# Optimization experiments

Hardware: AMD Instinct MI355X
Metric: run time of the kernel (lower is better)

The kernel has to match this reference:

```python
import jax, jax.numpy as jnp
import numpy as np

TAU, LBDA, THETA = 0.25, 0.15, 0.3
N_WARPS, N_ITERS = 1, 30
EPS = 1e-12  # GRAD_IS_ZERO

GAUSS = jnp.array([
    [0.000874, 0.006976, 0.01386, 0.006976, 0.000874],
    [0.006976, 0.0557, 0.110656, 0.0557, 0.006976],
    [0.01386, 0.110656, 0.219833, 0.110656, 0.01386],
    [0.006976, 0.0557, 0.110656, 0.0557, 0.006976],
    [0.000874, 0.006976, 0.01386, 0.006976, 0.000874]], dtype=jnp.float32)


def to_gray(x):  # [B,3,H,W] -> [B,1,H,W], BGR-style weights from repo
    w = jnp.array([0.114, 0.587, 0.299], x.dtype)
    return jnp.einsum('bchw,c->bhw', x, w)[:, None]


def normalize_pair(x1, x2):
    mn = jnp.minimum(x1.min(), x2.min())
    mx = jnp.maximum(x1.max(), x2.max())
    den = mx - mn
    return 255.0 * (x1 - mn) / den, 255.0 * (x2 - mn) / den


def gaussian_smooth(x):
    k = GAUSS[None, None].astype(x.dtype)
    return jax.lax.conv_general_dilated(x, k, (1, 1), 'SAME')


def centered_grad(x):  # central differences, one-sided at borders (scaled 0.5)
    dx = jnp.concatenate([0.5 * (x[..., 1:2] - x[..., 0:1]),
                          0.5 * (x[..., 2:] - x[..., :-2]),
                          0.5 * (x[..., -1:] - x[..., -2:-1])], axis=-1)
    dy = jnp.concatenate([0.5 * (x[..., 1:2, :] - x[..., 0:1, :]),
                          0.5 * (x[..., 2:, :] - x[..., :-2, :]),
                          0.5 * (x[..., -1:, :] - x[..., -2:-1, :])], axis=-2)
    return dx, dy


def fwd_grad(x):  # forward differences, zero at last col/row
    dx = jnp.concatenate([x[..., 1:] - x[..., :-1], jnp.zeros_like(x[..., :1])], axis=-1)
    dy = jnp.concatenate([x[..., 1:, :] - x[..., :-1, :], jnp.zeros_like(x[..., :1, :])], axis=-2)
    return dx, dy


def divergence(px, py):  # adjoint of fwd_grad (backward differences with boundary handling)
    xp = jnp.concatenate([jnp.zeros_like(px[..., :1]), px[..., :-1]], axis=-1)
    yp = jnp.concatenate([jnp.zeros_like(py[..., :1, :]), py[..., :-1, :]], axis=-2)
    dx = jnp.concatenate([xp[..., 1:] - xp[..., :-1], -xp[..., -1:]], axis=-1)
    dy = jnp.concatenate([yp[..., 1:, :] - yp[..., :-1, :], -yp[..., -1:, :]], axis=-2)
    return dx + dy


def warp(x, u, v):  # grid_sample bilinear, align_corners=True, zeros padding
    B, C, H, W = x.shape
    base_x = jnp.linspace(-1.0, 1.0, W)[None, None, :]
    base_y = jnp.linspace(-1.0, 1.0, H)[None, :, None]
    gx = base_x + 2.0 * u[:, 0] / W   # [B,H,W]
    gy = base_y + 2.0 * v[:, 0] / H
    ix = (gx + 1.0) * 0.5 * (W - 1)
    iy = (gy + 1.0) * 0.5 * (H - 1)
    ix0 = jnp.floor(ix); iy0 = jnp.floor(iy)
    wx = ix - ix0; wy = iy - iy0

    def gather(yy, xx):
        valid = (xx >= 0) & (xx <= W - 1) & (yy >= 0) & (yy <= H - 1)
        xi = jnp.clip(xx, 0, W - 1).astype(jnp.int32)
        yi = jnp.clip(yy, 0, H - 1).astype(jnp.int32)
        flat = (yi * W + xi).reshape(B, 1, H * W)
        g = jnp.take_along_axis(x.reshape(B, C, H * W), flat, axis=2).reshape(B, C, H, W)
        return g * valid[:, None].astype(x.dtype)

    return (gather(iy0, ix0) * ((1 - wx) * (1 - wy))[:, None]
            + gather(iy0, ix0 + 1) * (wx * (1 - wy))[:, None]
            + gather(iy0 + 1, ix0) * ((1 - wx) * wy)[:, None]
            + gather(iy0 + 1, ix0 + 1) * (wx * wy)[:, None])


def tvnet_scale(x1, x2, u1, u2):
    l_t = LBDA * THETA
    taut = TAU / THETA
    d2x, d2y = centered_grad(x2)
    p11 = jnp.zeros_like(x1); p12 = jnp.zeros_like(x1)
    p21 = jnp.zeros_like(x1); p22 = jnp.zeros_like(x1)
    rho = jnp.zeros_like(x1)
    for _ in range(N_WARPS):
        x2w = warp(x2, u1, u2)
        dxw = warp(d2x, u1, u2)
        dyw = warp(d2y, u1, u2)
        grad = dxw ** 2 + dyw ** 2 + EPS
        rho_c = x2w - dxw * u1 - dyw * u2 - x1

        def body(carry, _):
            u1, u2, p11, p12, p21, p22, _ = carry
            rho = rho_c + dxw * u1 + dyw * u2 + EPS
            th = l_t * grad
            m3 = (rho >= -th) & (rho <= th) & (grad > EPS)
            coef = (jnp.where(rho < -th, l_t, 0.0)
                    + jnp.where(rho > th, -l_t, 0.0)
                    + jnp.where(m3, -rho / grad, 0.0))
            v1 = coef * dxw + u1
            v2 = coef * dyw + u2
            u1n = v1 + THETA * divergence(p11, p12)
            u2n = v2 + THETA * divergence(p21, p22)
            u1x, u1y = fwd_grad(u1n)
            u2x, u2y = fwd_grad(u2n)
            ng1 = 1.0 + taut * jnp.sqrt(u1x ** 2 + u1y ** 2 + EPS)
            ng2 = 1.0 + taut * jnp.sqrt(u2x ** 2 + u2y ** 2 + EPS)
            p11n = (p11 + taut * u1x) / ng1
            p12n = (p12 + taut * u1y) / ng1
            p21n = (p21 + taut * u2x) / ng2
            p22n = (p22 + taut * u2y) / ng2
            return (u1n, u2n, p11n, p12n, p21n, p22n, rho), None

        (u1, u2, p11, p12, p21, p22, rho), _ = jax.lax.scan(
            body, (u1, u2, p11, p12, p21, p22, rho), None, length=N_ITERS)
    return u1, u2, rho


def setup_inputs() -> dict:
    key = jax.random.key(0)
    k1, k2 = jax.random.split(key)
    x1 = jax.random.uniform(k1, (8, 3, 256, 256), dtype=jnp.float32)
    x2 = jax.random.uniform(k2, (8, 3, 256, 256), dtype=jnp.float32)
    return {"x1": x1, "x2": x2}


def reference(x1, x2):
    g1 = to_gray(x1)
    g2 = to_gray(x2)
    n1, n2 = normalize_pair(g1, g2)
    s1 = gaussian_smooth(n1)
    s2 = gaussian_smooth(n2)
    u1 = jnp.zeros_like(s1)
    u2 = jnp.zeros_like(s1)
    u1, u2, rho = tvnet_scale(s1, s2, u1, u2)
    return jnp.concatenate([u1, u2, rho], axis=1)  # [B,3,H,W]
```

## Files before the change

kernel.cpp:

```cpp
#include <hip/hip_runtime.h>
#include <math.h>

typedef float v2f __attribute__((ext_vector_type(2)));
static __device__ __forceinline__ v2f v2(float a, float b){ v2f r; r.x=a; r.y=b; return r; }
#define PKFMA(a,b,c) __builtin_elementwise_fma((a),(b),(c))

#define HH 256
#define WW 256
#define BB 8
#define NPIX (BB*HH*WW)
#define HWPLANE (HH*WW)
#define EPSF 1e-12f

#define TS 32
#define HL 10
#define SS (TS + 2*HL)
#define SS2 (SS*SS)
#define NTH 1024
#define NC 3

#define GSS (TS + 6)
#define GSS2 (GSS*GSS)
#define S2S (TS + 2)
#define S2S2 (S2S*S2S)

constexpr float L_T   = (float)(0.15*0.3);
constexpr float TAUT  = (float)(0.25/0.3);
constexpr float THETA = 0.3f;

static __device__ __constant__ float GK[25] = {
  0.000874f, 0.006976f, 0.01386f,  0.006976f, 0.000874f,
  0.006976f, 0.0557f,   0.110656f, 0.0557f,   0.006976f,
  0.01386f,  0.110656f, 0.219833f, 0.110656f, 0.01386f,
  0.006976f, 0.0557f,   0.110656f, 0.0557f,   0.006976f,
  0.000874f, 0.006976f, 0.01386f,  0.006976f, 0.000874f };


__global__ void k_gray_minmax(const float* __restrict__ x1, const float* __restrict__ x2,
                              float* __restrict__ g1, float* __restrict__ g2,
                              unsigned int* __restrict__ mnmx) {
    __shared__ float smn[4], smx[4];
    float mn = 1e30f, mx = -1e30f;
    int stride = gridDim.x * blockDim.x;
    const int NV = 2*NPIX/4;
    for (int v = blockIdx.x*blockDim.x + threadIdx.x; v < NV; v += stride) {
        int img = v >> 17;
        int rem = v & (NPIX/4 - 1);
        const float* x = img ? x2 : x1;
        float* g = img ? g2 : g1;
        int b = rem >> 14;
        int pix = (rem & (HWPLANE/4 - 1)) << 2;
        const float* base = x + (size_t)b*3*HWPLANE + pix;
        float4 c0 = *(const float4*)(base);
        float4 c1 = *(const float4*)(base + HWPLANE);
        float4 c2 = *(const float4*)(base + 2*HWPLANE);
        float4 gr;
        gr.x = 0.114f*c0.x + 0.587f*c1.x + 0.299f*c2.x;
        gr.y = 0.114f*c0.y + 0.587f*c1.y + 0.299f*c2.y;
        gr.z = 0.114f*c0.z + 0.587f*c1.z + 0.299f*c2.z;
        gr.w = 0.114f*c0.w + 0.587f*c1.w + 0.299f*c2.w;
        *(float4*)(g + ((size_t)rem << 2)) = gr;
        mn = fminf(mn, fminf(fminf(gr.x, gr.y), fminf(gr.z, gr.w)));
        mx = fmaxf(mx, fmaxf(fmaxf(gr.x, gr.y), fmaxf(gr.z, gr.w)));
    }
    #pragma unroll
    for (int off = 32; off; off >>= 1) {
        mn = fminf(mn, __shfl_down(mn, off, 64));
        mx = fmaxf(mx, __shfl_down(mx, off, 64));
    }
    int wid = threadIdx.x >> 6;
    if ((threadIdx.x & 63) == 0) { smn[wid] = mn; smx[wid] = mx; }
    __syncthreads();
    if (threadIdx.x == 0) {
        mn = fminf(fminf(smn[0], smn[1]), fminf(smn[2], smn[3]));
        mx = fmaxf(fmaxf(smx[0], smx[1]), fmaxf(smx[2], smx[3]));
        atomicMin(&mnmx[0], __float_as_uint(mn));
        atomicMax((int*)&mnmx[1], (int)__float_as_uint(mx));
    }
}

__global__ void __launch_bounds__(256)
k_smooth_grad(const float* __restrict__ g1, const float* __restrict__ g2,
              const unsigned int* __restrict__ mnmx, float4* __restrict__ dxr) {
    __shared__ float gn1[GSS2], gn2[GSS2], s2L[S2S2];
    const int blk   = blockIdx.x;
    const int plane = blk >> 6;
    const int t     = blk & 63;
    const int oy0   = (t >> 3) << 5;
    const int ox0   = (t & 7) << 5;
    const int pbse  = plane * HWPLANE;
    const int tid   = threadIdx.x;

    const float mn  = __uint_as_float(mnmx[0]);
    const float inv = 255.0f / (__uint_as_float(mnmx[1]) - mn);

    for (int s = tid; s < GSS2; s += 256) {
        int sy = s / GSS, sx = s - sy*GSS;
        int gy = oy0 - 3 + sy, gx = ox0 - 3 + sx;
        bool im = (gx >= 0) & (gx < WW) & (gy >= 0) & (gy < HH);
        int gi = pbse + gy*WW + gx;
        gn1[s] = im ? (g1[gi] - mn)*inv : 0.f;
        gn2[s] = im ? (g2[gi] - mn)*inv : 0.f;
    }
    __syncthreads();

    for (int c = tid; c < S2S2; c += 256) {
        int sy = c / S2S, sx = c - sy*S2S;
        const float* gb = gn2 + sy*GSS + sx;
        float acc = 0.f;
        #pragma unroll
        for (int i = 0; i < 5; ++i)
            #pragma unroll
            for (int j = 0; j < 5; ++j)
                acc += gb[i*GSS + j] * GK[i*5 + j];
        s2L[c] = acc;
    }
    float s1r[4];
    #pragma unroll
    for (int i = 0; i < 4; ++i) {
        int c = tid + i*256;
        int oy = c >> 5, ox = c & 31;
        const float* gb = gn1 + (oy+1)*GSS + (ox+1);
        float acc = 0.f;
        #pragma unroll
        for (int ii = 0; ii < 5; ++ii)
            #pragma unroll
            for (int jj = 0; jj < 5; ++jj)
                acc += gb[ii*GSS + jj] * GK[ii*5 + jj];
        s1r[i] = acc;
    }
    __syncthreads();

    #pragma unroll
    for (int i = 0; i < 4; ++i) {
        int c = tid + i*256;
        int oy = c >> 5, ox = c & 31;
        int gy = oy0 + oy, gx = ox0 + ox;
        int sc = (oy+1)*S2S + (ox+1);
        float s2c = s2L[sc];
        float xp = (gx < WW-1) ? s2L[sc+1]    : s2c;
        float xm = (gx > 0)    ? s2L[sc-1]    : s2c;
        float yp = (gy < HH-1) ? s2L[sc+S2S]  : s2c;
        float ym = (gy > 0)    ? s2L[sc-S2S]  : s2c;
        dxr[pbse + gy*WW + gx] =
            make_float4(0.5f*(xp - xm), 0.5f*(yp - ym), s2c - s1r[i], 0.f);
    }
}

__global__ void __launch_bounds__(NTH)
k_iter10(float* __restrict__ F, float* __restrict__ out, int itbase) {
    const float4* DXR = (const float4*)F;
    const int j  = itbase / HL;
    const int rd = j & 1;
    const v2f* Ur  = (const v2f*)(F + (size_t)NPIX*(rd ? 12 : 6));
    const v2f* PAr = (const v2f*)(F + (size_t)NPIX*(rd ? 14 : 8));
    const v2f* PBr = (const v2f*)(F + (size_t)NPIX*(rd ? 16 : 10));
    v2f* Uw  = (v2f*)(F + (size_t)NPIX*(rd ? 6 : 12));
    v2f* PAw = (v2f*)(F + (size_t)NPIX*(rd ? 8 : 14));
    v2f* PBw = (v2f*)(F + (size_t)NPIX*(rd ? 10 : 16));

    __shared__ v2f u12[SS2];
    __shared__ v2f pa [SS2];
    __shared__ v2f pb [SS2];

    const int blk   = blockIdx.x;
    const int plane = blk >> 6;
    const int t     = blk & 63;
    const int gy0   = ((t >> 3) << 5) - HL;
    const int gx0   = ((t & 7) << 5) - HL;
    const int pbse  = plane * HWPLANE;
    const int tid   = threadIdx.x;
    const int sxmax = WW-1 - gx0;
    const int symax = HH-1 - gy0;

    int cc[NC];
    v2f dv[NC]; float rcv[NC];
    v2f ru[NC];
    v2f rpa[NC];
    v2f rpb[NC];

    #pragma unroll
    for (int i = 0; i < NC; ++i) {
        int s = tid + i*NTH;
        cc[i] = 0;
        dv[i] = v2(0.f, 0.f); rcv[i] = EPSF;
        ru[i] = v2(0.f, 0.f);
        rpa[i] = v2(0.f, 0.f); rpb[i] = v2(0.f, 0.f);
        if (s < SS2) {
            int sy = s / SS, sx = s - sy*SS;
            int gy = gy0 + sy, gx = gx0 + sx;
            bool im = (gx >= 0) & (gx < WW) & (gy >= 0) & (gy < HH);
            if (im) {
                int m  = min(min(sy-1, sx-1), min(SS-1-sy, SS-1-sx));
                int mp = min(m, min(SS-2-sy, SS-2-sx));
                int ku1 = max(m,  -1) + 1;
                int kp1 = max(mp, -1) + 1;
                cc[i] = (kp1 << 24) | (ku1 << 16) | (sy << 6) | sx;
                int gi = pbse + gy*WW + gx;
                float4 dvv = DXR[gi];
                dv[i] = v2(dvv.x, dvv.y); rcv[i] = dvv.z + EPSF;
                if (itbase) {
                    ru[i] = Ur[gi]; rpa[i] = PAr[gi]; rpb[i] = PBr[gi];
                }
            }
            u12[s] = ru[i];
            pa[s]  = rpa[i];
            pb[s]  = rpb[i];
        }
    }
    __syncthreads();

    #pragma unroll 1
    for (int k = 0; k < HL; ++k) {
        const bool it29 = (itbase + k == 29);

        #pragma unroll
        for (int i = 0; i < NC; ++i) {
            if (k >= ((cc[i] >> 16) & 0xFF)) continue;
            int s = tid + i*NTH;
            float rhov = fmaf(dv[i].x, ru[i].x, fmaf(dv[i].y, ru[i].y, rcv[i]));
            float grad = fmaf(dv[i].x, dv[i].x, fmaf(dv[i].y, dv[i].y, EPSF));
            float coef = fminf(fmaxf(-rhov * __builtin_amdgcn_rcpf(grad), -L_T), L_T);
            v2f pal = pa[s-1], pbu = pb[s-SS];
            v2f d  = (rpa[i] - pal) + (rpb[i] - pbu);
            v2f un = PKFMA(v2(THETA,THETA), d,
                           PKFMA(v2(coef,coef), dv[i], ru[i]));
            if (it29) {
                int sy = (cc[i] >> 6) & 63, sx = cc[i] & 63;
                if (sy >= HL && sy < HL+TS && sx >= HL && sx < HL+TS) {
                    float* o = out + (size_t)plane*3*HWPLANE + (gy0+sy)*WW + (gx0+sx);
                    o[0]         = un.x;
                    o[HWPLANE]   = un.y;
                    o[2*HWPLANE] = rhov;
                }
            } else {
                ru[i] = un;
                u12[s] = un;
            }
        }
        if (it29) return;
        __syncthreads();

        #pragma unroll
        for (int i = 0; i < NC; ++i) {
            if (k >= (int)((unsigned)cc[i] >> 24)) continue;
            int s = tid + i*NTH;
            int sy = (cc[i] >> 6) & 63, sx = cc[i] & 63;
            float fbm = (sx < sxmax) ? 1.f : 0.f;
            float fdm = (sy < symax) ? 1.f : 0.f;
            v2f ux = (u12[s+1]  - ru[i]) * fbm;
            v2f uy = (u12[s+SS] - ru[i]) * fdm;
            v2f q  = PKFMA(ux, ux, PKFMA(uy, uy, v2(EPSF,EPSF)));
            v2f sq = v2(__builtin_amdgcn_sqrtf(q.x), __builtin_amdgcn_sqrtf(q.y));
            v2f ng = PKFMA(v2(TAUT,TAUT), sq, v2(1.f,1.f));
            v2f r  = v2(__builtin_amdgcn_rcpf(ng.x), __builtin_amdgcn_rcpf(ng.y));
            rpa[i] = PKFMA(v2(TAUT,TAUT), ux, rpa[i]) * r;
            rpb[i] = PKFMA(v2(TAUT,TAUT), uy, rpb[i]) * r;
            pa[s] = rpa[i];
            pb[s] = rpb[i];
        }
        __syncthreads();
    }

    if (tid < TS*TS) {
        int oy = tid >> 5, ox = tid & 31;
        int ss = (HL+oy)*SS + (HL+ox);
        int gi = pbse + (gy0+HL+oy)*WW + (gx0+HL+ox);
        Uw[gi] = u12[ss]; PAw[gi] = pa[ss]; PBw[gi] = pb[ss];
    }
}

extern "C" void kernel_launch(void* const* d_in, const int* in_sizes, int n_in,
                              void* d_out, int out_size, void* d_ws, size_t ws_size,
                              hipStream_t stream) {
    const float* x1 = (const float*)d_in[0];
    const float* x2 = (const float*)d_in[1];
    float* out = (float*)d_out;

    char* ws = (char*)d_ws;
    unsigned int* mnmx = (unsigned int*)ws;
    float* F = (float*)(ws + 256);
    float4* dxr = (float4*)F;
    float*  g1  = F + 4*(size_t)NPIX;
    float*  g2  = F + 5*(size_t)NPIX;

    k_gray_minmax<<<dim3(512), dim3(256), 0, stream>>>(x1, x2, g1, g2, mnmx);
    k_smooth_grad<<<dim3(512), dim3(256), 0, stream>>>(g1, g2, mnmx, dxr);

    for (int itbase = 0; itbase < 30; itbase += HL)
        k_iter10<<<dim3(512), dim3(NTH), 0, stream>>>(F, out, itbase);
}
```

Baseline: 177.2 us.

## Store inter-launch state in fp16, precompute gradient reciprocal, write state from registers

The U, PA and PB state carried between the 10-iteration launches is now stored in global memory as half2 instead of float2, halving that traffic. The reciprocal of the squared image gradient is computed once in the setup kernel and packed into the unused fourth lane of the float4, so it no longer has to be recomputed every iteration. On the final inner step, owning threads write their results directly from registers, which drops the last barrier and the separate shared-memory copy-out. The fp16 state costs accuracy at each launch boundary and could push the output past the tolerance.

```diff
diff --git a/kernel.cpp b/kernel.cpp
--- a/kernel.cpp
+++ b/kernel.cpp
@@ -1,4 +1,5 @@
 #include <hip/hip_runtime.h>
+#include <hip/hip_fp16.h>
 #include <math.h>
 
 typedef float v2f __attribute__((ext_vector_type(2)));
@@ -18,6 +19,7 @@
 #define SS2 (SS*SS)
 #define NTH 1024
 #define NC 3
+#define OWNBIT (1<<12)
 
 #define GSS (TS + 6)
 #define GSS2 (GSS*GSS)
@@ -142,8 +144,10 @@
         float xm = (gx > 0)    ? s2L[sc-1]    : s2c;
         float yp = (gy < HH-1) ? s2L[sc+S2S]  : s2c;
         float ym = (gy > 0)    ? s2L[sc-S2S]  : s2c;
-        dxr[pbse + gy*WW + gx] =
-            make_float4(0.5f*(xp - xm), 0.5f*(yp - ym), s2c - s1r[i], 0.f);
+        float dx = 0.5f*(xp - xm), dy = 0.5f*(yp - ym);
+        float grad = fmaf(dx, dx, fmaf(dy, dy, EPSF));
+        float rgr  = __builtin_amdgcn_rcpf(grad);
+        dxr[pbse + gy*WW + gx] = make_float4(dx, dy, s2c - s1r[i], rgr);
     }
 }
 
@@ -152,12 +156,12 @@
     const float4* DXR = (const float4*)F;
     const int j  = itbase / HL;
     const int rd = j & 1;
-    const v2f* Ur  = (const v2f*)(F + (size_t)NPIX*(rd ? 12 : 6));
-    const v2f* PAr = (const v2f*)(F + (size_t)NPIX*(rd ? 14 : 8));
-    const v2f* PBr = (const v2f*)(F + (size_t)NPIX*(rd ? 16 : 10));
-    v2f* Uw  = (v2f*)(F + (size_t)NPIX*(rd ? 6 : 12));
-    v2f* PAw = (v2f*)(F + (size_t)NPIX*(rd ? 8 : 14));
-    v2f* PBw = (v2f*)(F + (size_t)NPIX*(rd ? 10 : 16));
+    const __half2* Ur  = (const __half2*)(F + (size_t)NPIX*(rd ? 12 : 6));
+    const __half2* PAr = (const __half2*)(F + (size_t)NPIX*(rd ? 14 : 8));
+    const __half2* PBr = (const __half2*)(F + (size_t)NPIX*(rd ? 16 : 10));
+    __half2* Uw  = (__half2*)(F + (size_t)NPIX*(rd ? 6 : 12));
+    __half2* PAw = (__half2*)(F + (size_t)NPIX*(rd ? 8 : 14));
+    __half2* PBw = (__half2*)(F + (size_t)NPIX*(rd ? 10 : 16));
 
     __shared__ v2f u12[SS2];
     __shared__ v2f pa [SS2];
@@ -174,7 +178,7 @@
     const int symax = HH-1 - gy0;
 
     int cc[NC];
-    v2f dv[NC]; float rcv[NC];
+    v2f dv[NC]; float rcv[NC], rgr[NC];
     v2f ru[NC];
     v2f rpa[NC];
     v2f rpb[NC];
@@ -183,7 +187,7 @@
     for (int i = 0; i < NC; ++i) {
         int s = tid + i*NTH;
         cc[i] = 0;
-        dv[i] = v2(0.f, 0.f); rcv[i] = EPSF;
+        dv[i] = v2(0.f, 0.f); rcv[i] = EPSF; rgr[i] = 0.f;
         ru[i] = v2(0.f, 0.f);
         rpa[i] = v2(0.f, 0.f); rpb[i] = v2(0.f, 0.f);
         if (s < SS2) {
@@ -195,12 +199,18 @@
                 int mp = min(m, min(SS-2-sy, SS-2-sx));
                 int ku1 = max(m,  -1) + 1;
                 int kp1 = max(mp, -1) + 1;
-                cc[i] = (kp1 << 24) | (ku1 << 16) | (sy << 6) | sx;
+                int own = (int)((sy >= HL) & (sy < HL+TS) & (sx >= HL) & (sx < HL+TS));
+                cc[i] = (kp1 << 24) | (ku1 << 16) | (own << 12) | (sy << 6) | sx;
                 int gi = pbse + gy*WW + gx;
                 float4 dvv = DXR[gi];
-                dv[i] = v2(dvv.x, dvv.y); rcv[i] = dvv.z + EPSF;
+                dv[i] = v2(dvv.x, dvv.y); rcv[i] = dvv.z + EPSF; rgr[i] = dvv.w;
                 if (itbase) {
-                    ru[i] = Ur[gi]; rpa[i] = PAr[gi]; rpb[i] = PBr[gi];
+                    float2 uv  = __half22float2(Ur[gi]);
+                    float2 pav = __half22float2(PAr[gi]);
+                    float2 pbv = __half22float2(PBr[gi]);
+                    ru[i]  = v2(uv.x,  uv.y);
+                    rpa[i] = v2(pav.x, pav.y);
+                    rpb[i] = v2(pbv.x, pbv.y);
                 }
             }
             u12[s] = ru[i];
@@ -212,22 +222,22 @@
 
     #pragma unroll 1
     for (int k = 0; k < HL; ++k) {
-        const bool it29 = (itbase + k == 29);
+        const bool lastk = (k == HL-1);
+        const bool it29  = (itbase + k == 29);
 
         #pragma unroll
         for (int i = 0; i < NC; ++i) {
             if (k >= ((cc[i] >> 16) & 0xFF)) continue;
             int s = tid + i*NTH;
             float rhov = fmaf(dv[i].x, ru[i].x, fmaf(dv[i].y, ru[i].y, rcv[i]));
-            float grad = fmaf(dv[i].x, dv[i].x, fmaf(dv[i].y, dv[i].y, EPSF));
-            float coef = fminf(fmaxf(-rhov * __builtin_amdgcn_rcpf(grad), -L_T), L_T);
+            float coef = fminf(fmaxf(-rhov * rgr[i], -L_T), L_T);
             v2f pal = pa[s-1], pbu = pb[s-SS];
             v2f d  = (rpa[i] - pal) + (rpb[i] - pbu);
             v2f un = PKFMA(v2(THETA,THETA), d,
                            PKFMA(v2(coef,coef), dv[i], ru[i]));
             if (it29) {
-                int sy = (cc[i] >> 6) & 63, sx = cc[i] & 63;
-                if (sy >= HL && sy < HL+TS && sx >= HL && sx < HL+TS) {
+                if (cc[i] & OWNBIT) {
+                    int sy = (cc[i] >> 6) & 63, sx = cc[i] & 63;
                     float* o = out + (size_t)plane*3*HWPLANE + (gy0+sy)*WW + (gx0+sx);
                     o[0]         = un.x;
                     o[HWPLANE]   = un.y;
@@ -236,6 +246,10 @@
             } else {
                 ru[i] = un;
                 u12[s] = un;
+                if (lastk && (cc[i] & OWNBIT)) {
+                    int sy = (cc[i] >> 6) & 63, sx = cc[i] & 63;
+                    Uw[pbse + (gy0+sy)*WW + (gx0+sx)] = __floats2half2_rn(un.x, un.y);
+                }
             }
         }
         if (it29) return;
@@ -256,17 +270,16 @@
             v2f r  = v2(__builtin_amdgcn_rcpf(ng.x), __builtin_amdgcn_rcpf(ng.y));
             rpa[i] = PKFMA(v2(TAUT,TAUT), ux, rpa[i]) * r;
             rpb[i] = PKFMA(v2(TAUT,TAUT), uy, rpb[i]) * r;
-            pa[s] = rpa[i];
-            pb[s] = rpb[i];
+            if (!lastk) {
+                pa[s] = rpa[i];
+                pb[s] = rpb[i];
+            } else if (cc[i] & OWNBIT) {
+                int gi = pbse + (gy0+sy)*WW + (gx0+sx);
+                PAw[gi] = __floats2half2_rn(rpa[i].x, rpa[i].y);
+                PBw[gi] = __floats2half2_rn(rpb[i].x, rpb[i].y);
+            }
         }
-        __syncthreads();
-    }
-
-    if (tid < TS*TS) {
-        int oy = tid >> 5, ox = tid & 31;
-        int ss = (HL+oy)*SS + (HL+ox);
-        int gi = pbse + (gy0+HL+oy)*WW + (gx0+HL+ox);
-        Uw[gi] = u12[ss]; PAw[gi] = pa[ss]; PBw[gi] = pb[ss];
+        if (!lastk) __syncthreads();
     }
 }
 
```

Result: faster. 164.8 us (-7.0%).
